# Performance work log

Measured on AMD Instinct MI355X. Metric: run time of the kernel, lower is better.

Reference implementation:

```python
import jax, jax.numpy as jnp
import numpy as np

HIDDEN = 384
HEADS = 8
HEAD_DIM = HIDDEN // HEADS
K_NN = 10
CLUSTER_SIZE = 256
KMEANS_ITERS = 50
LN_EPS = 1e-5


def layernorm(x, g, b):
    mu = x.mean(-1, keepdims=True)
    var = ((x - mu) ** 2).mean(-1, keepdims=True)
    return (x - mu) / jnp.sqrt(var + LN_EPS) * g + b


def mha(x, w_in, b_in, w_out, b_out, mask=None):
    # x: [L, C]; torch nn.MultiheadAttention math (eval mode, no dropout)
    L, C = x.shape
    qkv = x @ w_in.T + b_in                      # [L, 3C]
    q, k, v = jnp.split(qkv, 3, axis=-1)
    q = q.reshape(L, HEADS, HEAD_DIM)
    k = k.reshape(L, HEADS, HEAD_DIM)
    v = v.reshape(L, HEADS, HEAD_DIM)
    scores = jnp.einsum('lhd,mhd->hlm', q, k) / jnp.sqrt(jnp.float32(HEAD_DIM))
    if mask is not None:
        scores = jnp.where(mask[None], scores, -jnp.inf)
    attn = jax.nn.softmax(scores, axis=-1)
    out = jnp.einsum('hlm,mhd->lhd', attn, v).reshape(L, C)
    return out @ w_out.T + b_out


def attn_block(x, w_in, b_in, w_out, b_out, g, b, mask=None):
    # HierarchicalSelfAttention: residual MHA + LayerNorm
    return layernorm(x + mha(x, w_in, b_in, w_out, b_out, mask), g, b)


def cluster_labels(x, coords, weight_params, n_cluster):
    # mirrors the torch.no_grad() clustering block: fused cosine+spatial
    # similarity -> top-k kNN graph -> KMeans on row-normalized topk values.
    feats = x[0]
    co = coords[0]
    L = feats.shape[0]
    w = jax.nn.softmax(weight_params)
    fz = (feats - feats.mean(0)) / (feats.std(0, ddof=1) + 1e-6)
    fz = fz / jnp.clip(jnp.linalg.norm(fz, axis=1, keepdims=True), 1e-12)
    cz = (co - co.mean(0)) / (co.std(0, ddof=1) + 1e-6)
    cos = fz @ fz.T                                 # [L, L]
    sq = (cz ** 2).sum(1)
    d2 = jnp.maximum(sq[:, None] + sq[None, :] - 2.0 * (cz @ cz.T), 0.0)
    dist = jnp.sqrt(d2)
    sigma = dist.std(ddof=1) + 1e-6
    sim = w[0] * cos + w[1] * jnp.exp(-dist / sigma)
    vals, _ = jax.lax.top_k(sim, K_NN)              # [L, k]
    knn = vals / (vals.sum(1, keepdims=True) + 1e-6)
    # deterministic KMeans (fixed iters, evenly spaced init) on knn features
    init_idx = jnp.linspace(0, L - 1, n_cluster).astype(jnp.int32)
    centers0 = knn[init_idx]

    def body(_, centers):
        dd = ((knn[:, None, :] - centers[None]) ** 2).sum(-1)   # [L, nc]
        lab = jnp.argmin(dd, axis=1)
        sums = jax.ops.segment_sum(knn, lab, num_segments=n_cluster)
        cnt = jax.ops.segment_sum(jnp.ones((L,), knn.dtype), lab, num_segments=n_cluster)
        return jnp.where(cnt[:, None] > 0, sums / jnp.maximum(cnt, 1.0)[:, None], centers)

    centers = jax.lax.fori_loop(0, KMEANS_ITERS, body, centers0)
    dd = ((knn[:, None, :] - centers[None]) ** 2).sum(-1)
    return jnp.argmin(dd, axis=1)


def setup_inputs() -> dict:
    key = jax.random.key(0)
    ks = jax.random.split(key, 16)
    L, C = 4096, HIDDEN
    s = 0.02
    inp = {
        'x': jax.random.normal(ks[0], (1, L, C), jnp.float32),
        'coords': jax.random.uniform(ks[1], (1, L, 2), jnp.float32) * 100.0,
        'weight_params': jnp.array([0.8, 0.2], jnp.float32),
        'lw_in': jax.random.normal(ks[2], (3 * C, C), jnp.float32) * s,
        'lb_in': jnp.zeros((3 * C,), jnp.float32),
        'lw_out': jax.random.normal(ks[3], (C, C), jnp.float32) * s,
        'lb_out': jnp.zeros((C,), jnp.float32),
        'lg': jnp.ones((C,), jnp.float32),
        'lb': jnp.zeros((C,), jnp.float32),
        'gw_in': jax.random.normal(ks[4], (3 * C, C), jnp.float32) * s,
        'gb_in': jnp.zeros((3 * C,), jnp.float32),
        'gw_out': jax.random.normal(ks[5], (C, C), jnp.float32) * s,
        'gb_out': jnp.zeros((C,), jnp.float32),
        'gg': jnp.ones((C,), jnp.float32),
        'gb': jnp.zeros((C,), jnp.float32),
    }
    return inp


def reference(x, coords, weight_params, lw_in, lb_in, lw_out, lb_out, lg, lb,
              gw_in, gb_in, gw_out, gb_out, gg, gb):
    L = x.shape[1]
    n_cluster = max(1, L // CLUSTER_SIZE)
    labels = jax.lax.stop_gradient(
        cluster_labels(jax.lax.stop_gradient(x), coords, weight_params, n_cluster))
    # per-cluster local attention expressed as block mask over same-label pairs
    mask = labels[:, None] == labels[None, :]
    h = attn_block(x[0], lw_in, lb_in, lw_out, lb_out, lg, lb, mask)   # [L, C]
    cnt = jax.ops.segment_sum(jnp.ones((L,), h.dtype), labels, num_segments=n_cluster)
    reps = jax.ops.segment_sum(h, labels, num_segments=n_cluster) / jnp.maximum(cnt, 1.0)[:, None]
    reps = attn_block(reps, gw_in, gb_in, gw_out, gb_out, gg, gb)      # [nc, C]
    h = h + reps.mean(0, keepdims=True)
    return h[None]  # [1, L, C]
```

## Files before the change

### kernel.cpp

```cpp
#include <hip/hip_runtime.h>
#include <math.h>
#include <stdint.h>

typedef unsigned long long u64;

constexpr int L  = 4096;
constexpr int C  = 384;
constexpr int C3 = 1152;
constexpr int HD = 48;
constexpr int NCL = 16;
constexpr int KNN = 10;
constexpr int KM_ITERS = 50;

constexpr size_t AL(size_t x){ return (x + 255) & ~size_t(255); }
constexpr size_t OFF_AB    = 0;
constexpr size_t OFF_FZ    = OFF_AB;
constexpr size_t OFF_QKV   = OFF_AB;
constexpr size_t OFF_ATTN  = AL(OFF_AB    + sizeof(float)*L*C3);
constexpr size_t OFF_H     = AL(OFF_ATTN  + sizeof(float)*L*C);
constexpr size_t OFF_CZ    = AL(OFF_H     + sizeof(float)*L*C);
constexpr size_t OFF_SQ    = AL(OFF_CZ    + sizeof(double)*L*2);
constexpr size_t OFF_CM    = AL(OFF_SQ    + sizeof(double)*L);
constexpr size_t OFF_CD    = AL(OFF_CM    + sizeof(double)*C);
constexpr size_t OFF_CCM   = AL(OFF_CD    + sizeof(double)*C);
constexpr size_t OFF_CCD   = AL(OFF_CCM   + sizeof(double)*2);
constexpr size_t OFF_SP    = AL(OFF_CCD   + sizeof(double)*2);
constexpr size_t OFF_SP2   = AL(OFF_SP    + sizeof(double)*512);
constexpr size_t OFF_CONST = AL(OFF_SP2   + sizeof(double)*512);
constexpr size_t OFF_KNN   = AL(OFF_CONST + sizeof(double)*8);
constexpr size_t OFF_LBL   = AL(OFF_KNN   + sizeof(double)*L*KNN);
constexpr size_t OFF_ORD   = AL(OFF_LBL   + sizeof(int)*L);
constexpr size_t OFF_OFFS  = AL(OFF_ORD   + sizeof(int)*L);
constexpr size_t OFF_REPS  = AL(OFF_OFFS  + sizeof(int)*32);
constexpr size_t OFF_GQKV  = AL(OFF_REPS  + sizeof(float)*NCL*C);
constexpr size_t OFF_GATT  = AL(OFF_GQKV  + sizeof(float)*NCL*C3);
constexpr size_t OFF_GREP  = AL(OFF_GATT  + sizeof(float)*NCL*C);
constexpr size_t OFF_RMEAN = AL(OFF_GREP  + sizeof(float)*NCL*C);
constexpr size_t OFF_CTRL  = AL(OFF_RMEAN + sizeof(float)*C);

struct KCtrl {
  u64 sums[3][160];
  int cnt[3][16];
  int chg[3];
  int bar;
};
constexpr size_t CTRL_BYTES = sizeof(KCtrl);
constexpr double FXS = 4503599627370496.0;

#define SCOPE_AGENT __HIP_MEMORY_SCOPE_AGENT

__global__ void k_colstats(const float* __restrict__ x, const float* __restrict__ coords, char* ws){
  double* colm = (double*)(ws + OFF_CM);
  double* cold = (double*)(ws + OFF_CD);
  double* ccm  = (double*)(ws + OFF_CCM);
  double* ccd  = (double*)(ws + OFF_CCD);
  int b = blockIdx.x, t = threadIdx.x;
  __shared__ double red[256];
  __shared__ double muS[16];
  if (b < 24) {
    int co = t & 15, rg = t >> 4;
    int col = b*16 + co;
    double s = 0.0;
    for (int r = rg; r < L; r += 16) s += (double)x[r*C + col];
    red[t] = s; __syncthreads();
    for (int w = 8; w >= 1; w >>= 1){ if (rg < w) red[t] += red[t + w*16]; __syncthreads(); }
    if (rg == 0) muS[co] = red[co] / 4096.0;
    __syncthreads();
    double mu = muS[co];
    double ss = 0.0;
    for (int r = rg; r < L; r += 16){ double d = (double)x[r*C + col] - mu; ss += d * d; }
    red[t] = ss; __syncthreads();
    for (int w = 8; w >= 1; w >>= 1){ if (rg < w) red[t] += red[t + w*16]; __syncthreads(); }
    if (rg == 0){ colm[col] = mu; cold[col] = sqrt(red[co] / 4095.0) + 1e-6; }
  } else {
    int co = t & 1, rg = t >> 1;
    double s = 0.0;
    for (int r = rg; r < L; r += 128) s += (double)coords[r*2 + co];
    red[t] = s; __syncthreads();
    for (int w = 64; w >= 1; w >>= 1){ if (rg < w) red[t] += red[t + w*2]; __syncthreads(); }
    if (rg == 0) muS[co] = red[co] / 4096.0;
    __syncthreads();
    double mu = muS[co];
    double ss = 0.0;
    for (int r = rg; r < L; r += 128){ double d = (double)coords[r*2 + co] - mu; ss += d * d; }
    red[t] = ss; __syncthreads();
    for (int w = 64; w >= 1; w >>= 1){ if (rg < w) red[t] += red[t + w*2]; __syncthreads(); }
    if (rg == 0){ ccm[co] = mu; ccd[co] = sqrt(red[co] / 4095.0) + 1e-6; }
  }
}

__global__ void k_normalize(const float* __restrict__ x, const float* __restrict__ coords, char* ws){
  double* fz = (double*)(ws + OFF_FZ);
  double* cz = (double*)(ws + OFF_CZ);
  double* sq = (double*)(ws + OFF_SQ);
  const double* colm = (const double*)(ws + OFF_CM);
  const double* cold = (const double*)(ws + OFF_CD);
  const double* ccm  = (const double*)(ws + OFF_CCM);
  const double* ccd  = (const double*)(ws + OFF_CCD);
  int i = blockIdx.x, t = threadIdx.x;
  double z[3];
  #pragma unroll
  for (int q = 0; q < 3; q++){ int c = t + q*128; z[q] = ((double)x[i*C + c] - colm[c]) / cold[c]; }
  __shared__ double red[128];
  __shared__ double nrmS;
  double s = z[0]*z[0] + z[1]*z[1] + z[2]*z[2];
  red[t] = s; __syncthreads();
  for (int w = 64; w >= 1; w >>= 1){ if (t < w) red[t] += red[t + w]; __syncthreads(); }
  if (t == 0){ double n = sqrt(red[0]); nrmS = n > 1e-12 ? n : 1e-12; }
  __syncthreads();
  double n = nrmS;
  #pragma unroll
  for (int q = 0; q < 3; q++){ int c = t + q*128; fz[(size_t)i*C + c] = z[q] / n; }
  if (t == 0){
    #pragma clang fp contract(off)
    double c0 = ((double)coords[i*2 + 0] - ccm[0]) / ccd[0];
    double c1 = ((double)coords[i*2 + 1] - ccm[1]) / ccd[1];
    cz[i*2 + 0] = c0; cz[i*2 + 1] = c1;
    double p0 = c0*c0; double p1 = c1*c1;
    sq[i] = p0 + p1;
  }
}

__global__ void k_sigsum(char* ws){
  const double* cz = (const double*)(ws + OFF_CZ);
  const double* sq = (const double*)(ws + OFF_SQ);
  double* sp = (double*)(ws + OFF_SP);
  int b = blockIdx.x, t = threadIdx.x;
  double s = 0.0;
  const long long total = (long long)L * (long long)L;
  for (long long idx = (long long)b*256 + t; idx < total; idx += (long long)512*256){
    #pragma clang fp contract(off)
    int i = (int)(idx >> 12), j = (int)(idx & 4095);
    double p0 = cz[i*2] * cz[j*2];
    double p1 = cz[i*2+1] * cz[j*2+1];
    double g = p0 + p1;
    double d2 = (sq[i] + sq[j]) - 2.0*g;
    d2 = d2 > 0.0 ? d2 : 0.0;
    s += sqrt(d2);
  }
  __shared__ double r1[256];
  r1[t] = s; __syncthreads();
  for (int w = 128; w >= 1; w >>= 1){ if (t < w) r1[t] += r1[t+w]; __syncthreads(); }
  if (t == 0) sp[b] = r1[0];
}

__global__ void k_sigmean(char* ws){
  const double* sp = (const double*)(ws + OFF_SP);
  double* cst = (double*)(ws + OFF_CONST);
  int t = threadIdx.x;
  __shared__ double r1[256];
  double a = sp[t] + sp[256 + t];
  r1[t] = a; __syncthreads();
  for (int w = 128; w >= 1; w >>= 1){ if (t < w) r1[t] += r1[t+w]; __syncthreads(); }
  if (t == 0) cst[3] = r1[0] / ((double)L * (double)L);
}

__global__ void k_sigvar(char* ws){
  const double* cz = (const double*)(ws + OFF_CZ);
  const double* sq = (const double*)(ws + OFF_SQ);
  const double* cst = (const double*)(ws + OFF_CONST);
  double* sp2 = (double*)(ws + OFF_SP2);
  int b = blockIdx.x, t = threadIdx.x;
  double mean = cst[3];
  double s = 0.0;
  const long long total = (long long)L * (long long)L;
  for (long long idx = (long long)b*256 + t; idx < total; idx += (long long)512*256){
    #pragma clang fp contract(off)
    int i = (int)(idx >> 12), j = (int)(idx & 4095);
    double p0 = cz[i*2] * cz[j*2];
    double p1 = cz[i*2+1] * cz[j*2+1];
    double g = p0 + p1;
    double d2 = (sq[i] + sq[j]) - 2.0*g;
    d2 = d2 > 0.0 ? d2 : 0.0;
    double d = sqrt(d2) - mean;
    s += d * d;
  }
  __shared__ double r1[256];
  r1[t] = s; __syncthreads();
  for (int w = 128; w >= 1; w >>= 1){ if (t < w) r1[t] += r1[t+w]; __syncthreads(); }
  if (t == 0) sp2[b] = r1[0];
}

__global__ void k_consts(const float* __restrict__ wp, char* ws){
  const double* sp2 = (const double*)(ws + OFF_SP2);
  double* cst = (double*)(ws + OFF_CONST);
  int t = threadIdx.x;
  __shared__ double r1[256];
  double a = sp2[t] + sp2[256 + t];
  r1[t] = a; __syncthreads();
  for (int w = 128; w >= 1; w >>= 1){ if (t < w) r1[t] += r1[t+w]; __syncthreads(); }
  if (t == 0){
    double N = (double)L * (double)L;
    double var = r1[0] / (N - 1.0);
    cst[0] = sqrt(var) + 1e-6;
    double a0 = (double)wp[0], a1 = (double)wp[1];
    double m = a0 > a1 ? a0 : a1;
    double e0 = exp(a0 - m), e1 = exp(a1 - m);
    cst[1] = e0 / (e0 + e1);
    cst[2] = e1 / (e0 + e1);
  }
}

__launch_bounds__(512, 1)
__global__ void k_simtopk(char* ws){
  const double* __restrict__ fz = (const double*)(ws + OFF_FZ);
  const double* __restrict__ cz = (const double*)(ws + OFF_CZ);
  const double* __restrict__ sq = (const double*)(ws + OFF_SQ);
  const double* __restrict__ cst = (const double*)(ws + OFF_CONST);
  double* knn = (double*)(ws + OFF_KNN);
  __shared__ double simt[16*513];
  __shared__ double Acz[32], Asq[16];
  int t = threadIdx.x;
  int i0 = blockIdx.x * 16;
  if (t < 16){ Asq[t] = sq[i0 + t]; Acz[2*t] = cz[(i0+t)*2]; Acz[2*t+1] = cz[(i0+t)*2+1]; }
  double sigma = cst[0], w0 = cst[1], w1 = cst[2];
  double t10[10];
  #pragma unroll
  for (int q = 0; q < 10; q++) t10[q] = -INFINITY;
  const double2* aj = (const double2*)(fz + (size_t)i0*C);
  __syncthreads();

  for (int p = 0; p < 8; p++){
    int j = p*512 + t;
    double acc[16];
    #pragma unroll
    for (int r = 0; r < 16; r++) acc[r] = 0.0;
    const double2* bj = (const double2*)(fz + (size_t)j*C);
    for (int k2 = 0; k2 < 192; k2++){
      double2 b = bj[k2];
      #pragma unroll
      for (int r = 0; r < 16; r++){
        double2 a = aj[(size_t)r*192 + k2];
        acc[r] += a.x*b.x + a.y*b.y;
      }
    }
    {
      #pragma clang fp contract(off)
      double cj0 = cz[j*2], cj1 = cz[j*2+1], sj = sq[j];
      for (int r = 0; r < 16; r++){
        double p0 = Acz[2*r]*cj0; double p1 = Acz[2*r+1]*cj1;
        double g = p0 + p1;
        double d2 = (Asq[r] + sj) - 2.0*g;
        d2 = d2 > 0.0 ? d2 : 0.0;
        double dst = sqrt(d2);
        double e = exp(-dst / sigma);
        double u0 = w0*acc[r]; double u1 = w1*e;
        simt[r*513 + t] = u0 + u1;
      }
    }
    __syncthreads();
    if (t < 128){
      int r = t & 15, g = t >> 4;
      const double* row = &simt[r*513 + g*64];
      for (int q = 0; q < 64; q++){
        double v = row[q];
        if (v > t10[9]){
          t10[9] = v;
          #pragma unroll
          for (int u = 9; u >= 1; --u){
            if (t10[u] > t10[u-1]){ double tmp = t10[u-1]; t10[u-1] = t10[u]; t10[u] = tmp; }
          }
        }
      }
    }
    __syncthreads();
  }
  if (t < 128){
    int r = t & 15, g = t >> 4;
    #pragma unroll
    for (int q = 0; q < 10; q++) simt[(r*8+g)*10 + q] = t10[q];
  }
  __syncthreads();
  if (t < 16){
    double f10[10];
    #pragma unroll
    for (int q = 0; q < 10; q++) f10[q] = -INFINITY;
    for (int g = 0; g < 8; g++){
      for (int q = 0; q < 10; q++){
        double v = simt[(t*8+g)*10 + q];
        if (v > f10[9]){
          f10[9] = v;
          #pragma unroll
          for (int u = 9; u >= 1; --u){
            if (f10[u] > f10[u-1]){ double tmp = f10[u-1]; f10[u-1] = f10[u]; f10[u] = tmp; }
          }
        }
      }
    }
    double s = 0.0;
    #pragma unroll
    for (int q = 0; q < 10; q++) s += f10[q];
    s = s + 1e-6;
    #pragma unroll
    for (int q = 0; q < 10; q++) knn[(size_t)(i0 + t)*KNN + q] = f10[q] / s;
  }
}

__device__ __forceinline__ void gbar(int* bar, int target){
  __syncthreads();
  if (threadIdx.x == 0){
    __hip_atomic_fetch_add(bar, 1, __ATOMIC_ACQ_REL, SCOPE_AGENT);
    while (__hip_atomic_load(bar, __ATOMIC_ACQUIRE, SCOPE_AGENT) < target){
      __builtin_amdgcn_s_sleep(1);
    }
  }
  __syncthreads();
}

__launch_bounds__(512, 1)
__global__ void k_kmeans(char* ws){
  const double* knn = (const double*)(ws + OFF_KNN);
  int* labels = (int*)(ws + OFF_LBL);
  KCtrl* ct = (KCtrl*)(ws + OFF_CTRL);
  int t = threadIdx.x, b = blockIdx.x;
  int P = b*512 + t;
  double x[10];
  #pragma unroll
  for (int d = 0; d < 10; d++) x[d] = knn[(size_t)P*KNN + d];
  __shared__ double cen[160];
  __shared__ u64 lsum[160];
  __shared__ int lcnt[16];
  __shared__ int lchg;
  if (t < 160) cen[t] = knn[(size_t)(273*(t/10))*KNN + (t % 10)];
  __syncthreads();
  int prev = -1, label = 0;
  int it = 0;
  for (; it < KM_ITERS; ++it){
    if (t < 160) lsum[t] = 0;
    if (t < 16) lcnt[t] = 0;
    if (t == 0) lchg = 0;
    __syncthreads();
    double best = INFINITY; int bi = 0;
    for (int c = 0; c < 16; ++c){
      #pragma clang fp contract(off)
      double dd = 0.0;
      #pragma unroll
      for (int d = 0; d < 10; ++d){ double df = x[d] - cen[c*10 + d]; double s2 = df*df; dd = dd + s2; }
      if (dd < best){ best = dd; bi = c; }
    }
    label = bi;
    #pragma unroll
    for (int d = 0; d < 10; d++){
      long long q = llrint(x[d] * FXS);
      atomicAdd(&lsum[bi*10 + d], (u64)q);
    }
    atomicAdd(&lcnt[bi], 1);
    u64 mb = __ballot(label != prev);
    if (((t & 63) == 0) && mb) atomicAdd(&lchg, (int)__popcll(mb));
    prev = label;
    __syncthreads();
    int slot = it % 3;
    if (t < 160){
      u64 pv = lsum[t];
      if (pv) __hip_atomic_fetch_add(&ct->sums[slot][t], pv, __ATOMIC_RELAXED, SCOPE_AGENT);
    }
    if (t < 16){
      int pc = lcnt[t];
      if (pc) __hip_atomic_fetch_add(&ct->cnt[slot][t], pc, __ATOMIC_RELAXED, SCOPE_AGENT);
    }
    if (t == 0 && lchg) __hip_atomic_fetch_add(&ct->chg[slot], lchg, __ATOMIC_RELAXED, SCOPE_AGENT);
    gbar(&ct->bar, 8*(it+1));
    int chg = __hip_atomic_load(&ct->chg[slot], __ATOMIC_RELAXED, SCOPE_AGENT);
    int zslot = (it + 2) % 3;
    if (t < 160){
      u64 sv = __hip_atomic_load(&ct->sums[slot][t], __ATOMIC_RELAXED, SCOPE_AGENT);
      int cc = __hip_atomic_load(&ct->cnt[slot][t/10], __ATOMIC_RELAXED, SCOPE_AGENT);
      double s = (double)(long long)sv * (1.0 / FXS);
      double cd = (double)cc;
      double nc = s / (cd > 1.0 ? cd : 1.0);
      if (cc > 0) cen[t] = nc;
      __hip_atomic_store(&ct->sums[zslot][t], (u64)0, __ATOMIC_RELAXED, SCOPE_AGENT);
    }
    if (t < 16) __hip_atomic_store(&ct->cnt[zslot][t], 0, __ATOMIC_RELAXED, SCOPE_AGENT);
    if (t == 0) __hip_atomic_store(&ct->chg[zslot], 0, __ATOMIC_RELAXED, SCOPE_AGENT);
    __syncthreads();
    if (chg == 0) break;
  }
  if (it == KM_ITERS){
    double best = INFINITY; int bi = 0;
    for (int c = 0; c < 16; ++c){
      #pragma clang fp contract(off)
      double dd = 0.0;
      #pragma unroll
      for (int d = 0; d < 10; ++d){ double df = x[d] - cen[c*10 + d]; double s2 = df*df; dd = dd + s2; }
      if (dd < best){ best = dd; bi = c; }
    }
    label = bi;
  }
  labels[P] = label;
}

__global__ void k_order(char* ws){
  const int* labels = (const int*)(ws + OFF_LBL);
  int* order = (int*)(ws + OFF_ORD);
  int* offs  = (int*)(ws + OFF_OFFS);
  int t = threadIdx.x;
  __shared__ int cnt[16];
  volatile __shared__ int base[17];
  int my = 0;
  for (int ch = 0; ch < 64; ch++){
    int l = labels[ch*64 + t];
    for (int c = 0; c < 16; c++){
      u64 m = __ballot(l == c);
      if (t == c) my += (int)__popcll(m);
    }
  }
  if (t < 16) cnt[t] = my;
  __syncthreads();
  if (t == 0){
    int a = 0;
    for (int c = 0; c < 16; c++){ base[c] = a; a += cnt[c]; }
    base[16] = a;
    for (int c = 0; c < 17; c++) offs[c] = base[c];
  }
  __syncthreads();
  u64 lower = (t == 0) ? 0ull : ((1ull << t) - 1ull);
  for (int ch = 0; ch < 64; ch++){
    int i = ch*64 + t;
    int l = labels[i];
    for (int c = 0; c < 16; c++){
      u64 m = __ballot(l == c);
      int bc = base[c];
      if (l == c){ int pos = bc + (int)__popcll(m & lower); order[pos] = i; }
      if (t == c) base[c] = bc + (int)__popcll(m);
    }
  }
}

__launch_bounds__(384, 1)
__global__ void k_qkv(const float* __restrict__ x, const float* __restrict__ w_in,
                      const float* __restrict__ b_in, char* ws){
  float* qkv = (float*)(ws + OFF_QKV);
  int b = blockIdx.x, t = threadIdx.x;
  int r0 = b*8;
  __shared__ __align__(16) float xs[8*384];
  for (int idx = t; idx < 8*384; idx += 384) xs[idx] = x[r0*C + idx];
  __syncthreads();
  for (int og = 0; og < 3; og++){
    int o = og*384 + t;
    const float* wr = w_in + (size_t)o*C;
    float acc[8];
    #pragma unroll
    for (int r = 0; r < 8; r++) acc[r] = 0.f;
    for (int k = 0; k < 384; k += 4){
      float4 wv = *(const float4*)(wr + k);
      #pragma unroll
      for (int r = 0; r < 8; r++){
        const float4 xv = *(const float4*)(&xs[r*384 + k]);
        acc[r] += xv.x*wv.x + xv.y*wv.y + xv.z*wv.z + xv.w*wv.w;
      }
    }
    float bias = b_in[o];
    #pragma unroll
    for (int r = 0; r < 8; r++) qkv[(size_t)(r0+r)*C3 + o] = acc[r] + bias;
  }
}

__launch_bounds__(256, 1)
__global__ void k_cattn(char* ws){
  const float* qkv = (const float*)(ws + OFF_QKV);
  const int* order = (const int*)(ws + OFF_ORD);
  const int* offs  = (const int*)(ws + OFF_OFFS);
  float* attn = (float*)(ws + OFF_ATTN);
  int c = blockIdx.x, yb = blockIdx.y;
  int tid = threadIdx.x;
  int w = tid >> 6, lane = tid & 63;
  int off = offs[c];
  int n = offs[c+1] - off;
  if (yb*4 >= n) return;
  __shared__ __align__(16) float qs[4][384];
  __shared__ __align__(16) float Kt[64][49];
  __shared__ __align__(16) float Vt[64][49];
  int srow = tid >> 2;
  int sd0  = (tid & 3) * 12;
  for (int q0 = yb*4; q0 < n; q0 += 256){
    int qi = q0 + w;
    bool act = (qi < n);
    int r = 0;
    if (act){
      r = order[off + qi];
      for (int idx = lane; idx < 384; idx += 64) qs[w][idx] = qkv[(size_t)r*C3 + idx];
    }
    for (int h = 0; h < 8; h++){
      float m = -INFINITY, lsum = 0.f, acc = 0.f;
      for (int t0 = 0; t0 < n; t0 += 64){
        int nt = (n - t0 < 64) ? (n - t0) : 64;
        __syncthreads();
        if (srow < nt){
          int mr = order[off + t0 + srow];
          const float* kp = qkv + (size_t)mr*C3 + 384 + h*HD + sd0;
          const float* vp = qkv + (size_t)mr*C3 + 768 + h*HD + sd0;
          #pragma unroll
          for (int q = 0; q < 12; q += 4){
            *(float4*)&Kt[srow][sd0 + q] = *(const float4*)(kp + q);
            *(float4*)&Vt[srow][sd0 + q] = *(const float4*)(vp + q);
          }
        }
        __syncthreads();
        if (act){
          float s = -INFINITY;
          if (lane < nt){
            const float* qh = &qs[w][h*HD];
            float dot = 0.f;
            #pragma unroll
            for (int d = 0; d < 48; d++) dot += qh[d] * Kt[lane][d];
            s = dot / 6.92820323027551f;
          }
          float cm = s;
          #pragma unroll
          for (int d = 32; d >= 1; d >>= 1) cm = fmaxf(cm, __shfl_xor(cm, d));
          float nm = fmaxf(m, cm);
          float alpha = expf(m - nm);
          float p = (lane < nt) ? expf(s - nm) : 0.f;
          float cs = p;
          #pragma unroll
          for (int d = 32; d >= 1; d >>= 1) cs += __shfl_xor(cs, d);
          lsum = lsum*alpha + cs;
          acc *= alpha;
          for (int jj = 0; jj < nt; jj++){
            float pv = __shfl(p, jj);
            if (lane < 48) acc += pv * Vt[jj][lane];
          }
          m = nm;
        }
      }
      if (act && lane < 48) attn[(size_t)r*C + h*HD + lane] = acc / lsum;
    }
  }
}

__launch_bounds__(384, 1)
__global__ void k_outln(const float* __restrict__ x, const float* __restrict__ w_out,
                        const float* __restrict__ b_out, const float* __restrict__ g,
                        const float* __restrict__ bb, char* ws){
  const float* attn = (const float*)(ws + OFF_ATTN);
  float* h = (float*)(ws + OFF_H);
  int b = blockIdx.x, t = threadIdx.x;
  int r0 = b*8;
  __shared__ __align__(16) float as[8*384];
  __shared__ float ov[8*384];
  __shared__ float red[8*48];
  __shared__ float stats[16];
  for (int idx = t; idx < 8*384; idx += 384) as[idx] = attn[(size_t)r0*C + idx];
  __syncthreads();
  const float* wr = w_out + (size_t)t*C;
  float acc[8];
  #pragma unroll
  for (int r = 0; r < 8; r++) acc[r] = 0.f;
  for (int k = 0; k < 384; k += 4){
    float4 wv = *(const float4*)(wr + k);
    #pragma unroll
    for (int r = 0; r < 8; r++){
      const float4 av = *(const float4*)(&as[r*384 + k]);
      acc[r] += av.x*wv.x + av.y*wv.y + av.z*wv.z + av.w*wv.w;
    }
  }
  float bias = b_out[t];
  #pragma unroll
  for (int r = 0; r < 8; r++){
    float v = acc[r] + bias + x[(size_t)(r0+r)*C + t];
    ov[r*384 + t] = v;
  }
  __syncthreads();
  int rr = t & 7, ii = t >> 3;
  float ps = 0.f;
  for (int j = ii; j < 384; j += 48) ps += ov[rr*384 + j];
  red[rr*48 + ii] = ps; __syncthreads();
  if (t < 8){ float s = 0.f; for (int q = 0; q < 48; q++) s += red[t*48 + q]; stats[t] = s / 384.f; }
  __syncthreads();
  float mu = stats[rr];
  float pv = 0.f;
  for (int j = ii; j < 384; j += 48){ float d = ov[rr*384 + j] - mu; pv += d*d; }
  red[rr*48 + ii] = pv; __syncthreads();
  if (t < 8){ float s = 0.f; for (int q = 0; q < 48; q++) s += red[t*48 + q]; stats[8 + t] = s / 384.f; }
  __syncthreads();
  #pragma unroll
  for (int r = 0; r < 8; r++){
    float mu2 = stats[r], var = stats[8 + r];
    float v = ov[r*384 + t];
    h[(size_t)(r0+r)*C + t] = (v - mu2) / sqrtf(var + 1e-5f) * g[t] + bb[t];
  }
}

__global__ void k_reps(char* ws){
  const float* h = (const float*)(ws + OFF_H);
  const int* order = (const int*)(ws + OFF_ORD);
  const int* offs  = (const int*)(ws + OFF_OFFS);
  float* reps = (float*)(ws + OFF_REPS);
  int c = blockIdx.x, t = threadIdx.x;
  int o0 = offs[c], o1 = offs[c+1];
  float acc = 0.f;
  for (int idx = o0; idx < o1; idx++){ int r = order[idx]; acc += h[(size_t)r*C + t]; }
  float cntf = (float)(o1 - o0);
  reps[c*C + t] = acc / fmaxf(cntf, 1.f);
}

__global__ void k_gqkv(const float* __restrict__ gw_in, const float* __restrict__ gb_in, char* ws){
  const float* reps = (const float*)(ws + OFF_REPS);
  float* gqkv = (float*)(ws + OFF_GQKV);
  int c = blockIdx.x / 3, og = blockIdx.x % 3;
  int t = threadIdx.x;
  __shared__ __align__(16) float rs[384];
  rs[t] = reps[c*C + t]; __syncthreads();
  int o = og*384 + t;
  const float* wr = gw_in + (size_t)o*C;
  float acc = 0.f;
  for (int k = 0; k < 384; k += 4){
    float4 wv = *(const float4*)(wr + k);
    const float4 rv = *(const float4*)(&rs[k]);
    acc += rv.x*wv.x + rv.y*wv.y + rv.z*wv.z + rv.w*wv.w;
  }
  gqkv[c*C3 + o] = acc + gb_in[o];
}

__global__ void k_gattn(char* ws){
  const float* gq = (const float*)(ws + OFF_GQKV);
  float* ga = (float*)(ws + OFF_GATT);
  int c = blockIdx.x, lane = threadIdx.x;
  __shared__ float sc[16], pr[16];
  for (int h = 0; h < 8; h++){
    if (lane < 16){
      float dot = 0.f;
      const float* qv = gq + c*C3 + h*HD;
      const float* kv = gq + lane*C3 + 384 + h*HD;
      for (int d = 0; d < 48; d++) dot += qv[d]*kv[d];
      sc[lane] = dot / 6.92820323027551f;
    }
    __threadfence_block();
    if (lane == 0){
      float mx = -INFINITY;
      for (int j = 0; j < 16; j++) mx = fmaxf(mx, sc[j]);
      float sum = 0.f;
      for (int j = 0; j < 16; j++){ float e = expf(sc[j] - mx); pr[j] = e; sum += e; }
      for (int j = 0; j < 16; j++) pr[j] /= sum;
    }
    __threadfence_block();
    if (lane < 48){
      float acc = 0.f;
      for (int j = 0; j < 16; j++) acc += pr[j] * gq[j*C3 + 768 + h*HD + lane];
      ga[c*C + h*HD + lane] = acc;
    }
    __threadfence_block();
  }
}

__global__ void k_goutln(const float* __restrict__ gw_out, const float* __restrict__ gb_out,
                         const float* __restrict__ gg, const float* __restrict__ gb2, char* ws){
  const float* ga = (const float*)(ws + OFF_GATT);
  const float* reps = (const float*)(ws + OFF_REPS);
  float* grep = (float*)(ws + OFF_GREP);
  int c = blockIdx.x, t = threadIdx.x;
  __shared__ __align__(16) float as[384];
  __shared__ float ov[384];
  __shared__ float red[64];
  __shared__ float st[2];
  as[t] = ga[c*C + t]; __syncthreads();
  const float* wr = gw_out + (size_t)t*C;
  float acc = 0.f;
  for (int k = 0; k < 384; k += 4){
    float4 wv = *(const float4*)(wr + k);
    const float4 av = *(const float4*)(&as[k]);
    acc += av.x*wv.x + av.y*wv.y + av.z*wv.z + av.w*wv.w;
  }
  float v = acc + gb_out[t] + reps[c*C + t];
  ov[t] = v; __syncthreads();
  if (t < 64){ float s = 0.f; for (int j = t; j < 384; j += 64) s += ov[j]; red[t] = s; }
  __syncthreads();
  if (t == 0){ float s = 0.f; for (int q = 0; q < 64; q++) s += red[q]; st[0] = s / 384.f; }
  __syncthreads();
  float mu = st[0];
  if (t < 64){ float s = 0.f; for (int j = t; j < 384; j += 64){ float d = ov[j]-mu; s += d*d; } red[t] = s; }
  __syncthreads();
  if (t == 0){ float s = 0.f; for (int q = 0; q < 64; q++) s += red[q]; st[1] = s / 384.f; }
  __syncthreads();
  grep[c*C + t] = (v - mu) / sqrtf(st[1] + 1e-5f) * gg[t] + gb2[t];
}

__global__ void k_repmean(char* ws){
  const float* grep = (const float*)(ws + OFF_GREP);
  float* rm = (float*)(ws + OFF_RMEAN);
  int t = threadIdx.x;
  float s = 0.f;
  for (int c = 0; c < 16; c++) s += grep[c*C + t];
  rm[t] = s / 16.f;
}

__global__ void k_final(char* ws, float* __restrict__ out){
  const float4* h = (const float4*)(ws + OFF_H);
  const float4* rm = (const float4*)(ws + OFF_RMEAN);
  int idx = blockIdx.x*256 + threadIdx.x;
  float4 hv = h[idx];
  float4 rv = rm[idx % 96];
  ((float4*)out)[idx] = make_float4(hv.x + rv.x, hv.y + rv.y, hv.z + rv.z, hv.w + rv.w);
}

extern "C" void kernel_launch(void* const* d_in, const int* in_sizes, int n_in,
                              void* d_out, int out_size, void* d_ws, size_t ws_size,
                              hipStream_t stream){
  (void)in_sizes; (void)n_in; (void)out_size; (void)ws_size;
  const float* x      = (const float*)d_in[0];
  const float* coords = (const float*)d_in[1];
  const float* wp     = (const float*)d_in[2];
  const float* lw_in  = (const float*)d_in[3];
  const float* lb_in  = (const float*)d_in[4];
  const float* lw_out = (const float*)d_in[5];
  const float* lb_out = (const float*)d_in[6];
  const float* lg     = (const float*)d_in[7];
  const float* lb     = (const float*)d_in[8];
  const float* gw_in  = (const float*)d_in[9];
  const float* gb_in  = (const float*)d_in[10];
  const float* gw_out = (const float*)d_in[11];
  const float* gb_out = (const float*)d_in[12];
  const float* gg     = (const float*)d_in[13];
  const float* gb     = (const float*)d_in[14];
  char* ws = (char*)d_ws;

  hipMemsetAsync(ws + OFF_CTRL, 0, AL(CTRL_BYTES), stream);
  hipLaunchKernelGGL(k_colstats,  dim3(25),       dim3(256), 0, stream, x, coords, ws);
  hipLaunchKernelGGL(k_normalize, dim3(4096),     dim3(128), 0, stream, x, coords, ws);
  hipLaunchKernelGGL(k_sigsum,    dim3(512),      dim3(256), 0, stream, ws);
  hipLaunchKernelGGL(k_sigmean,   dim3(1),        dim3(256), 0, stream, ws);
  hipLaunchKernelGGL(k_sigvar,    dim3(512),      dim3(256), 0, stream, ws);
  hipLaunchKernelGGL(k_consts,    dim3(1),        dim3(256), 0, stream, wp, ws);
  hipLaunchKernelGGL(k_simtopk,   dim3(256),      dim3(512), 0, stream, ws);
  hipLaunchKernelGGL(k_kmeans,    dim3(8),        dim3(512), 0, stream, ws);
  hipLaunchKernelGGL(k_order,     dim3(1),        dim3(64),  0, stream, ws);
  hipLaunchKernelGGL(k_qkv,       dim3(512),      dim3(384), 0, stream, x, lw_in, lb_in, ws);
  hipLaunchKernelGGL(k_cattn,     dim3(16, 64),   dim3(256), 0, stream, ws);
  hipLaunchKernelGGL(k_outln,     dim3(512),      dim3(384), 0, stream, x, lw_out, lb_out, lg, lb, ws);
  hipLaunchKernelGGL(k_reps,      dim3(16),       dim3(384), 0, stream, ws);
  hipLaunchKernelGGL(k_gqkv,      dim3(48),       dim3(384), 0, stream, gw_in, gb_in, ws);
  hipLaunchKernelGGL(k_gattn,     dim3(16),       dim3(64),  0, stream, ws);
  hipLaunchKernelGGL(k_goutln,    dim3(16),       dim3(384), 0, stream, gw_out, gb_out, gg, gb, ws);
  hipLaunchKernelGGL(k_repmean,   dim3(1),        dim3(384), 0, stream, ws);
  hipLaunchKernelGGL(k_final,     dim3(1536),     dim3(256), 0, stream, ws, (float*)d_out);
}
```

Measured before the change: 2.789 ms.

## Compute similarity top-k in fp32 then rescore candidates in fp64

Replaces the fp64 similarity-matrix plus top-k kernel with an fp32 version. The fp32 kernel stages the query rows in LDS, splits the columns across two blocks, and keeps 20 candidate indices per half. A new rescore kernel recomputes those 40 candidates per row in fp64 and selects the final top-10 to rebuild the knn features. The aim is to avoid the slow fp64 dense dot products. The risk is that fp32 rounding could drop a true top-10 neighbour from the candidate set.

```diff
diff --git a/kernel.cpp b/kernel.cpp
--- a/kernel.cpp
+++ b/kernel.cpp
@@ -11,12 +11,14 @@
 constexpr int NCL = 16;
 constexpr int KNN = 10;
 constexpr int KM_ITERS = 50;
+constexpr int NCAND = 20;
 
 constexpr size_t AL(size_t x){ return (x + 255) & ~size_t(255); }
 constexpr size_t OFF_AB    = 0;
 constexpr size_t OFF_FZ    = OFF_AB;
 constexpr size_t OFF_QKV   = OFF_AB;
 constexpr size_t OFF_ATTN  = AL(OFF_AB    + sizeof(float)*L*C3);
+constexpr size_t OFF_FZ32  = OFF_ATTN;
 constexpr size_t OFF_H     = AL(OFF_ATTN  + sizeof(float)*L*C);
 constexpr size_t OFF_CZ    = AL(OFF_H     + sizeof(float)*L*C);
 constexpr size_t OFF_SQ    = AL(OFF_CZ    + sizeof(double)*L*2);
@@ -45,6 +47,8 @@
   int bar;
 };
 constexpr size_t CTRL_BYTES = sizeof(KCtrl);
+constexpr size_t OFF_PTOP  = AL(OFF_CTRL + AL(CTRL_BYTES));
+constexpr size_t OFF_PIDX  = AL(OFF_PTOP + sizeof(float)*L*2*NCAND);
 constexpr double FXS = 4503599627370496.0;
 
 #define SCOPE_AGENT __HIP_MEMORY_SCOPE_AGENT
@@ -91,6 +95,7 @@
 
 __global__ void k_normalize(const float* __restrict__ x, const float* __restrict__ coords, char* ws){
   double* fz = (double*)(ws + OFF_FZ);
+  float* fz32 = (float*)(ws + OFF_FZ32);
   double* cz = (double*)(ws + OFF_CZ);
   double* sq = (double*)(ws + OFF_SQ);
   const double* colm = (const double*)(ws + OFF_CM);
@@ -110,7 +115,12 @@
   __syncthreads();
   double n = nrmS;
   #pragma unroll
-  for (int q = 0; q < 3; q++){ int c = t + q*128; fz[(size_t)i*C + c] = z[q] / n; }
+  for (int q = 0; q < 3; q++){
+    int c = t + q*128;
+    double v = z[q] / n;
+    fz[(size_t)i*C + c] = v;
+    fz32[(size_t)i*C + c] = (float)v;
+  }
   if (t == 0){
     #pragma clang fp contract(off)
     double c0 = ((double)coords[i*2 + 0] - ccm[0]) / ccd[0];
@@ -201,98 +211,159 @@
   }
 }
 
-__launch_bounds__(512, 1)
-__global__ void k_simtopk(char* ws){
+__launch_bounds__(512, 4)
+__global__ void k_simtopk32(char* ws){
+  const float* __restrict__ fz32 = (const float*)(ws + OFF_FZ32);
+  const double* __restrict__ cz = (const double*)(ws + OFF_CZ);
+  const double* __restrict__ sq = (const double*)(ws + OFF_SQ);
+  const double* __restrict__ cst = (const double*)(ws + OFF_CONST);
+  float* ptv = (float*)(ws + OFF_PTOP);
+  int*   pti = (int*)(ws + OFF_PIDX);
+  __shared__ __align__(16) float As[16*384];
+  __shared__ float sc[16*513];
+  __shared__ float Acz[32], Asq[16];
+  int t = threadIdx.x;
+  int i0 = blockIdx.x * 16;
+  int jbase = blockIdx.y * 2048;
+  for (int idx = t; idx < 16*384; idx += 512) As[idx] = fz32[(size_t)i0*C + idx];
+  if (t < 16){ Asq[t] = (float)sq[i0+t]; Acz[2*t] = (float)cz[(i0+t)*2]; Acz[2*t+1] = (float)cz[(i0+t)*2+1]; }
+  float sigma = (float)cst[0], w0 = (float)cst[1], w1 = (float)cst[2];
+  int j0 = jbase + t;
+  float acc[16][4];
+  #pragma unroll
+  for (int r = 0; r < 16; r++){ acc[r][0]=0.f; acc[r][1]=0.f; acc[r][2]=0.f; acc[r][3]=0.f; }
+  __syncthreads();
+
+  const float4* b0p = (const float4*)(fz32 + (size_t)(j0       )*C);
+  const float4* b1p = (const float4*)(fz32 + (size_t)(j0 +  512)*C);
+  const float4* b2p = (const float4*)(fz32 + (size_t)(j0 + 1024)*C);
+  const float4* b3p = (const float4*)(fz32 + (size_t)(j0 + 1536)*C);
+  for (int k4 = 0; k4 < 96; k4++){
+    float4 b0 = b0p[k4], b1 = b1p[k4], b2 = b2p[k4], b3 = b3p[k4];
+    #pragma unroll
+    for (int r = 0; r < 16; r++){
+      const float4 a = *(const float4*)(&As[r*384 + k4*4]);
+      acc[r][0] += a.x*b0.x + a.y*b0.y + a.z*b0.z + a.w*b0.w;
+      acc[r][1] += a.x*b1.x + a.y*b1.y + a.z*b1.z + a.w*b1.w;
+      acc[r][2] += a.x*b2.x + a.y*b2.y + a.z*b2.z + a.w*b2.w;
+      acc[r][3] += a.x*b3.x + a.y*b3.y + a.z*b3.z + a.w*b3.w;
+    }
+  }
+
+  float t10[10]; int i10[10];
+  #pragma unroll
+  for (int q = 0; q < 10; q++){ t10[q] = -INFINITY; i10[q] = 0; }
+
+  for (int jj = 0; jj < 4; jj++){
+    int j = j0 + jj*512;
+    float czj0 = (float)cz[j*2], czj1 = (float)cz[j*2+1], sj = (float)sq[j];
+    #pragma unroll
+    for (int r = 0; r < 16; r++){
+      float d2 = (Asq[r] + sj) - 2.0f*(Acz[2*r]*czj0 + Acz[2*r+1]*czj1);
+      d2 = fmaxf(d2, 0.f);
+      sc[r*513 + t] = w0*acc[r][jj] + w1*expf(-sqrtf(d2)/sigma);
+    }
+    __syncthreads();
+    if (t < 128){
+      int r = t & 15, g = t >> 4;
+      int jb2 = jbase + jj*512 + g*64;
+      const float* row = &sc[r*513 + g*64];
+      for (int q = 0; q < 64; q++){
+        float v = row[q];
+        if (v > t10[9]){
+          t10[9] = v; i10[9] = jb2 + q;
+          #pragma unroll
+          for (int u = 9; u >= 1; --u){
+            if (t10[u] > t10[u-1]){
+              float tv = t10[u-1]; t10[u-1] = t10[u]; t10[u] = tv;
+              int ti = i10[u-1]; i10[u-1] = i10[u]; i10[u] = ti;
+            }
+          }
+        }
+      }
+    }
+    __syncthreads();
+  }
+  float* lval = sc;
+  int*   lidx = ((int*)sc) + 1280;
+  if (t < 128){
+    int r = t & 15, g = t >> 4;
+    #pragma unroll
+    for (int q = 0; q < 10; q++){ lval[(r*8+g)*10 + q] = t10[q]; lidx[(r*8+g)*10 + q] = i10[q]; }
+  }
+  __syncthreads();
+  if (t < 16){
+    int ptr[8];
+    #pragma unroll
+    for (int g = 0; g < 8; g++) ptr[g] = 0;
+    for (int pop = 0; pop < NCAND; pop++){
+      float best = -INFINITY; int bg = 0;
+      #pragma unroll
+      for (int g = 0; g < 8; g++){
+        float v = (ptr[g] < 10) ? lval[(t*8+g)*10 + ptr[g]] : -INFINITY;
+        if (v > best){ best = v; bg = g; }
+      }
+      int bi = 0;
+      #pragma unroll
+      for (int g = 0; g < 8; g++){
+        if (bg == g){ bi = lidx[(t*8+g)*10 + ptr[g]]; ptr[g]++; }
+      }
+      size_t o = ((size_t)(i0 + t)*2 + blockIdx.y)*NCAND + pop;
+      ptv[o] = best; pti[o] = bi;
+    }
+  }
+}
+
+__global__ void k_rescore(char* ws){
   const double* __restrict__ fz = (const double*)(ws + OFF_FZ);
   const double* __restrict__ cz = (const double*)(ws + OFF_CZ);
   const double* __restrict__ sq = (const double*)(ws + OFF_SQ);
   const double* __restrict__ cst = (const double*)(ws + OFF_CONST);
+  const int* __restrict__ pti = (const int*)(ws + OFF_PIDX);
   double* knn = (double*)(ws + OFF_KNN);
-  __shared__ double simt[16*513];
-  __shared__ double Acz[32], Asq[16];
-  int t = threadIdx.x;
-  int i0 = blockIdx.x * 16;
-  if (t < 16){ Asq[t] = sq[i0 + t]; Acz[2*t] = cz[(i0+t)*2]; Acz[2*t+1] = cz[(i0+t)*2+1]; }
-  double sigma = cst[0], w0 = cst[1], w1 = cst[2];
-  double t10[10];
-  #pragma unroll
-  for (int q = 0; q < 10; q++) t10[q] = -INFINITY;
-  const double2* aj = (const double2*)(fz + (size_t)i0*C);
-  __syncthreads();
-
-  for (int p = 0; p < 8; p++){
-    int j = p*512 + t;
-    double acc[16];
-    #pragma unroll
-    for (int r = 0; r < 16; r++) acc[r] = 0.0;
-    const double2* bj = (const double2*)(fz + (size_t)j*C);
-    for (int k2 = 0; k2 < 192; k2++){
-      double2 b = bj[k2];
-      #pragma unroll
-      for (int r = 0; r < 16; r++){
-        double2 a = aj[(size_t)r*192 + k2];
-        acc[r] += a.x*b.x + a.y*b.y;
-      }
-    }
+  int wv = threadIdx.x >> 6, lane = threadIdx.x & 63;
+  int i = blockIdx.x*4 + wv;
+  double simv = -INFINITY;
+  if (lane < 2*NCAND){
+    int j = pti[(size_t)i*2*NCAND + lane];
+    const double* ar = fz + (size_t)i*C;
+    const double* br = fz + (size_t)j*C;
+    double d0 = 0.0, d1 = 0.0;
+    for (int k = 0; k < C; k += 2){ d0 += ar[k]*br[k]; d1 += ar[k+1]*br[k+1]; }
+    double dot = d0 + d1;
     {
       #pragma clang fp contract(off)
-      double cj0 = cz[j*2], cj1 = cz[j*2+1], sj = sq[j];
-      for (int r = 0; r < 16; r++){
-        double p0 = Acz[2*r]*cj0; double p1 = Acz[2*r+1]*cj1;
-        double g = p0 + p1;
-        double d2 = (Asq[r] + sj) - 2.0*g;
-        d2 = d2 > 0.0 ? d2 : 0.0;
-        double dst = sqrt(d2);
-        double e = exp(-dst / sigma);
-        double u0 = w0*acc[r]; double u1 = w1*e;
-        simt[r*513 + t] = u0 + u1;
+      double p0 = cz[i*2] * cz[j*2];
+      double p1 = cz[i*2+1] * cz[j*2+1];
+      double g = p0 + p1;
+      double d2 = (sq[i] + sq[j]) - 2.0*g;
+      d2 = d2 > 0.0 ? d2 : 0.0;
+      double dst = sqrt(d2);
+      double e = exp(-dst / cst[0]);
+      double u0 = cst[1]*dot; double u1 = cst[2]*e;
+      simv = u0 + u1;
+    }
+  }
+  double f10[10];
+  #pragma unroll
+  for (int q = 0; q < 10; q++) f10[q] = -INFINITY;
+  for (int c2 = 0; c2 < 2*NCAND; c2++){
+    double v = __shfl(simv, c2);
+    if (v > f10[9]){
+      f10[9] = v;
+      #pragma unroll
+      for (int u = 9; u >= 1; --u){
+        if (f10[u] > f10[u-1]){ double tmp = f10[u-1]; f10[u-1] = f10[u]; f10[u] = tmp; }
       }
     }
-    __syncthreads();
-    if (t < 128){
-      int r = t & 15, g = t >> 4;
-      const double* row = &simt[r*513 + g*64];
-      for (int q = 0; q < 64; q++){
-        double v = row[q];
-        if (v > t10[9]){
-          t10[9] = v;
-          #pragma unroll
-          for (int u = 9; u >= 1; --u){
-            if (t10[u] > t10[u-1]){ double tmp = t10[u-1]; t10[u-1] = t10[u]; t10[u] = tmp; }
-          }
-        }
-      }
-    }
-    __syncthreads();
-  }
-  if (t < 128){
-    int r = t & 15, g = t >> 4;
-    #pragma unroll
-    for (int q = 0; q < 10; q++) simt[(r*8+g)*10 + q] = t10[q];
-  }
-  __syncthreads();
-  if (t < 16){
-    double f10[10];
-    #pragma unroll
-    for (int q = 0; q < 10; q++) f10[q] = -INFINITY;
-    for (int g = 0; g < 8; g++){
-      for (int q = 0; q < 10; q++){
-        double v = simt[(t*8+g)*10 + q];
-        if (v > f10[9]){
-          f10[9] = v;
-          #pragma unroll
-          for (int u = 9; u >= 1; --u){
-            if (f10[u] > f10[u-1]){ double tmp = f10[u-1]; f10[u-1] = f10[u]; f10[u] = tmp; }
-          }
-        }
-      }
-    }
+  }
+  if (lane == 0){
     double s = 0.0;
     #pragma unroll
     for (int q = 0; q < 10; q++) s += f10[q];
     s = s + 1e-6;
     #pragma unroll
-    for (int q = 0; q < 10; q++) knn[(size_t)(i0 + t)*KNN + q] = f10[q] / s;
+    for (int q = 0; q < 10; q++) knn[(size_t)i*KNN + q] = f10[q] / s;
   }
 }
 
@@ -722,7 +793,8 @@
   hipLaunchKernelGGL(k_sigmean,   dim3(1),        dim3(256), 0, stream, ws);
   hipLaunchKernelGGL(k_sigvar,    dim3(512),      dim3(256), 0, stream, ws);
   hipLaunchKernelGGL(k_consts,    dim3(1),        dim3(256), 0, stream, wp, ws);
-  hipLaunchKernelGGL(k_simtopk,   dim3(256),      dim3(512), 0, stream, ws);
+  hipLaunchKernelGGL(k_simtopk32, dim3(256, 2),   dim3(512), 0, stream, ws);
+  hipLaunchKernelGGL(k_rescore,   dim3(1024),     dim3(256), 0, stream, ws);
   hipLaunchKernelGGL(k_kmeans,    dim3(8),        dim3(512), 0, stream, ws);
   hipLaunchKernelGGL(k_order,     dim3(1),        dim3(64),  0, stream, ws);
   hipLaunchKernelGGL(k_qkv,       dim3(512),      dim3(384), 0, stream, x, lw_in, lb_in, ws);
```

Result: slower. 3.746 ms (+34.3%).
